# Kernel optimization log

Measured on AMD Instinct MI355X. Metric: run time of the kernel, lower is better.

## Reference

```python
import jax, jax.numpy as jnp
import numpy as np

NEG_INF = -1000000000.0
INPUT_SIZE = 1024
HIDDEN_SIZE = 64
B, S = 8, 2048


def setup_inputs() -> dict:
    key = jax.random.key(0)
    ks = jax.random.split(key, 8)
    scale = 1.0 / np.sqrt(INPUT_SIZE)
    inp = {
        "input": jax.random.normal(ks[0], (B, S, INPUT_SIZE), dtype=jnp.float32),
        "mask": jax.random.randint(ks[1], (B, S, S), 0, 2, dtype=jnp.int32),
        "W_q": jax.random.uniform(ks[2], (HIDDEN_SIZE, INPUT_SIZE), jnp.float32, -scale, scale),
        "b_q": jax.random.uniform(ks[3], (HIDDEN_SIZE,), jnp.float32, -scale, scale),
        "W_k": jax.random.uniform(ks[4], (HIDDEN_SIZE, INPUT_SIZE), jnp.float32, -scale, scale),
        "b_k": jax.random.uniform(ks[5], (HIDDEN_SIZE,), jnp.float32, -scale, scale),
        "W_v": jax.random.uniform(ks[6], (HIDDEN_SIZE, INPUT_SIZE), jnp.float32, -scale, scale),
        "b_v": jax.random.uniform(ks[7], (HIDDEN_SIZE,), jnp.float32, -scale, scale),
    }
    return inp


def reference(input, mask, W_q, b_q, W_k, b_k, W_v, b_v):
    inv_sqrt_d = 1.0 / np.sqrt(HIDDEN_SIZE)
    # Q/K/V projections: torch Linear is x @ W.T + b
    q = jnp.einsum('bsi,hi->bsh', input, W_q) + b_q  # (B,S,H)
    k = jnp.einsum('bsi,hi->bsh', input, W_k) + b_k
    v = jnp.einsum('bsi,hi->bsh', input, W_v) + b_v
    scores = jnp.einsum('bqh,bkh->bqk', q, k) * inv_sqrt_d  # (B,S,S)
    scores = jnp.where(mask == 0, NEG_INF, scores)
    probs = jax.nn.softmax(scores, axis=-1)
    return jnp.einsum('bqk,bkh->bqh', probs, v)  # (B,S,H)
```

## Files before the change

### kernel.cpp

```cpp
#include <hip/hip_runtime.h>

typedef __bf16 bf16;
typedef bf16 bf16x4 __attribute__((ext_vector_type(4)));
typedef bf16 bf16x8 __attribute__((ext_vector_type(8)));
typedef float floatx4 __attribute__((ext_vector_type(4)));
typedef unsigned int u32;
typedef unsigned long long u64;

#define B_ 8
#define S_ 2048
#define I_ 1024
#define H_ 64

__device__ __forceinline__ void async_cp16(bf16* lds_base, const bf16* g_base, int lane) {
    __builtin_amdgcn_global_load_lds(
        (const __attribute__((address_space(1))) u32*)(g_base + lane * 8),
        (__attribute__((address_space(3))) u32*)lds_base, 16, 0, 0);
}

__global__ void conv_w(const float* __restrict__ Wq, const float* __restrict__ bq,
                       const float* __restrict__ Wk, const float* __restrict__ bk,
                       const float* __restrict__ Wv, const float* __restrict__ bv,
                       bf16* __restrict__ Wc2, float* __restrict__ bc) {
    int idx = blockIdx.x * 256 + threadIdx.x;
    int n = idx >> 10, i = idx & 1023;
    float v;
    if (n < 64)       v = Wq[n * I_ + i] * 0.125f;
    else if (n < 128) v = Wk[(n - 64) * I_ + i];
    else              v = Wv[(n - 128) * I_ + i];
    int s = i >> 7, kl = i & 127;
    Wc2[(size_t)s * 26112 + n * 136 + kl] = (bf16)v;
    if (idx < 192) {
        float bb = (idx < 64) ? bq[idx] * 0.125f
                 : (idx < 128) ? bk[idx - 64] : bv[idx - 128];
        bc[idx] = bb;
    }
}

__global__ __launch_bounds__(256, 2) void qkv_gemm(const float* __restrict__ X,
                                                   const bf16* __restrict__ Wc2,
                                                   const float* __restrict__ bc,
                                                   bf16* __restrict__ Qd,
                                                   bf16* __restrict__ Kd2,
                                                   bf16* __restrict__ Vt2) {
    __shared__ __align__(16) bf16 Xs[32 * 136];
    __shared__ __align__(16) bf16 Ws[26112];

    int tid = threadIdx.x;
    int w = tid >> 6, lane = tid & 63;
    int n = lane & 15, g = lane >> 4;
    int m0 = blockIdx.x * 32;
    int mt = w & 1, nh = (w >> 1) * 96;

    floatx4 zero4 = {0.0f, 0.0f, 0.0f, 0.0f};
    floatx4 acc[6];
#pragma unroll
    for (int t = 0; t < 6; ++t) acc[t] = zero4;

    int xrow = tid >> 3, xcb = (tid & 7) * 16;
    const float* xsrc = X + (size_t)(m0 + xrow) * I_ + xcb;
    bf16* xdst = Xs + xrow * 136 + xcb;

    for (int s = 0; s < 8; ++s) {
        const float* xp = xsrc + s * 128;
        float4 x0 = *(const float4*)(xp);
        float4 x1 = *(const float4*)(xp + 4);
        float4 x2 = *(const float4*)(xp + 8);
        float4 x3 = *(const float4*)(xp + 12);
#pragma unroll
        for (int i = 0; i < 13; ++i) {
            int inst = i * 4 + w;
            if (inst < 51)
                async_cp16(Ws + inst * 512, Wc2 + (size_t)s * 26112 + inst * 512, lane);
        }
        bf16x8 b0, b1;
        b0[0] = (bf16)x0.x; b0[1] = (bf16)x0.y; b0[2] = (bf16)x0.z; b0[3] = (bf16)x0.w;
        b0[4] = (bf16)x1.x; b0[5] = (bf16)x1.y; b0[6] = (bf16)x1.z; b0[7] = (bf16)x1.w;
        b1[0] = (bf16)x2.x; b1[1] = (bf16)x2.y; b1[2] = (bf16)x2.z; b1[3] = (bf16)x2.w;
        b1[4] = (bf16)x3.x; b1[5] = (bf16)x3.y; b1[6] = (bf16)x3.z; b1[7] = (bf16)x3.w;
        *(bf16x8*)xdst = b0;
        *(bf16x8*)(xdst + 8) = b1;
        __syncthreads();

#pragma unroll
        for (int ks = 0; ks < 4; ++ks) {
            bf16x8 xa = *(bf16x8*)(Xs + (mt * 16 + n) * 136 + ks * 32 + g * 8);
#pragma unroll
            for (int nt = 0; nt < 6; ++nt) {
                bf16x8 wb = *(bf16x8*)(Ws + (nh + nt * 16 + n) * 136 + ks * 32 + g * 8);
                acc[nt] = __builtin_amdgcn_mfma_f32_16x16x32_bf16(xa, wb, acc[nt], 0, 0, 0);
            }
        }
        __syncthreads();
    }

    int b = m0 >> 11;
    int sb = (m0 & 2047) + mt * 16 + g * 4;
#pragma unroll
    for (int nt = 0; nt < 6; ++nt) {
        int ng = nh + nt * 16 + n;
        float bias = bc[ng];
        if (ng < 64) {
#pragma unroll
            for (int r = 0; r < 4; ++r)
                Qd[(size_t)(b * S_ + sb + r) * H_ + ng] = (bf16)(acc[nt][r] + bias);
        } else if (ng < 128) {
            int hc = (ng - 64) >> 3, j = (ng - 64) & 7;
#pragma unroll
            for (int r = 0; r < 4; ++r)
                Kd2[((size_t)(b * 8 + hc) * S_ + sb + r) * 8 + j] = (bf16)(acc[nt][r] + bias);
        } else {
            int hh = ng - 128, kc = sb >> 3, jj = sb & 7;
            bf16x4 pk;
#pragma unroll
            for (int r = 0; r < 4; ++r) pk[r] = (bf16)(acc[nt][r] + bias);
            *(bf16x4*)(Vt2 + ((size_t)(b * 256 + kc) * 64 + hh) * 8 + jj) = pk;
        }
    }
}

__global__ __launch_bounds__(256, 4) void attn(const bf16* __restrict__ Qd,
                                               const bf16* __restrict__ Kd2,
                                               const bf16* __restrict__ Vt2,
                                               const int* __restrict__ mask,
                                               float* __restrict__ po,
                                               float* __restrict__ pl) {
    __shared__ __align__(16) bf16 regA[8704];
    __shared__ __align__(16) bf16 Vs[16 * 528];
    __shared__ __align__(16) u32 bfm[64][4];

    int tid = threadIdx.x;
    int w = tid >> 6, lane = tid & 63;
    int n = lane & 15, g = lane >> 4;
    int bid = blockIdx.x;
    int ksp = bid & 3;
    int qt = (bid >> 2) & 31;
    int b = bid >> 7;
    int q0 = qt * 64;

    const bf16* qptr = Qd + (size_t)(b * S_ + q0 + w * 16 + n) * H_ + g * 8;
    bf16x8 qa0 = *(const bf16x8*)qptr;
    bf16x8 qa1 = *(const bf16x8*)(qptr + 32);

    floatx4 zero4 = {0.0f, 0.0f, 0.0f, 0.0f};
    floatx4 o[4];
#pragma unroll
    for (int t = 0; t < 4; ++t) o[t] = zero4;
    float l_i[4] = {0.0f, 0.0f, 0.0f, 0.0f};

    const int* msl = mask + (size_t)(b * S_ + q0 + w * 16) * S_ + lane;

    for (int kt = ksp * 4; kt < ksp * 4 + 4; ++kt) {
        int mv[16][2];
#pragma unroll
        for (int rr = 0; rr < 16; ++rr)
#pragma unroll
            for (int c = 0; c < 2; ++c)
                mv[rr][c] = msl[(size_t)rr * S_ + kt * 128 + c * 64];
#pragma unroll
        for (int j = 0; j < 4; ++j) {
            int hc = w * 2 + (j >> 1), p = j & 1;
            async_cp16(regA + hc * 1040 + p * 512,
                       Kd2 + ((size_t)(b * 8 + hc) * S_ + kt * 128 + p * 64) * 8, lane);
        }
#pragma unroll
        for (int j = 0; j < 4; ++j) {
            int kcl = w * 4 + j;
            async_cp16(Vs + kcl * 528,
                       Vt2 + ((size_t)(b * 256 + kt * 16 + kcl) * 64) * 8, lane);
        }
#pragma unroll
        for (int rr = 0; rr < 16; ++rr)
#pragma unroll
            for (int c = 0; c < 2; ++c) {
                u64 bits = __ballot(mv[rr][c] != 0);
                if (lane == 0) {
                    bfm[w * 16 + rr][c * 2]     = (u32)bits;
                    bfm[w * 16 + rr][c * 2 + 1] = (u32)(bits >> 32);
                }
            }
        __syncthreads();

        u32 mq[4][4];
#pragma unroll
        for (int r = 0; r < 4; ++r) {
            uint4 t4 = *(const uint4*)&bfm[w * 16 + g * 4 + r][0];
            mq[r][0] = t4.x; mq[r][1] = t4.y; mq[r][2] = t4.z; mq[r][3] = t4.w;
        }

        floatx4 s[8];
#pragma unroll
        for (int nt = 0; nt < 8; ++nt) {
            floatx4 a = zero4;
            a = __builtin_amdgcn_mfma_f32_16x16x32_bf16(
                    qa0, *(const bf16x8*)(regA + g * 1040 + (nt * 16 + n) * 8), a, 0, 0, 0);
            a = __builtin_amdgcn_mfma_f32_16x16x32_bf16(
                    qa1, *(const bf16x8*)(regA + (4 + g) * 1040 + (nt * 16 + n) * 8), a, 0, 0, 0);
            s[nt] = a;
        }

#pragma unroll
        for (int r = 0; r < 4; ++r)
#pragma unroll
            for (int nt = 0; nt < 8; ++nt) {
                float e = __expf(s[nt][r]);
                bool bit = (mq[r][nt >> 1] >> ((nt & 1) * 16 + n)) & 1u;
                float p = bit ? e : 0.0f;
                s[nt][r] = p;
                l_i[r] += p;
            }
        __syncthreads();

#pragma unroll
        for (int r = 0; r < 4; ++r)
#pragma unroll
            for (int nt = 0; nt < 8; ++nt)
                regA[(w * 16 + g * 4 + r) * 136 + nt * 16 + n] = (bf16)s[nt][r];
        __syncthreads();

#pragma unroll
        for (int k0 = 0; k0 < 4; ++k0) {
            bf16x8 pa = *(bf16x8*)(regA + (w * 16 + n) * 136 + k0 * 32 + g * 8);
#pragma unroll
            for (int ht = 0; ht < 4; ++ht) {
                bf16x8 vb = *(bf16x8*)(Vs + (k0 * 4 + g) * 528 + (ht * 16 + n) * 8);
                o[ht] = __builtin_amdgcn_mfma_f32_16x16x32_bf16(pa, vb, o[ht], 0, 0, 0);
            }
        }
        __syncthreads();
    }

#pragma unroll
    for (int r = 0; r < 4; ++r)
#pragma unroll
        for (int off = 1; off < 16; off <<= 1)
            l_i[r] += __shfl_xor(l_i[r], off, 64);

    float* pb = po + (size_t)bid * 4096;
#pragma unroll
    for (int ht = 0; ht < 4; ++ht)
#pragma unroll
        for (int r = 0; r < 4; ++r)
            pb[(w * 16 + g * 4 + r) * 64 + ht * 16 + n] = o[ht][r];
    if (n == 0) {
#pragma unroll
        for (int r = 0; r < 4; ++r)
            pl[(size_t)bid * 64 + w * 16 + g * 4 + r] = l_i[r];
    }
}

__global__ __launch_bounds__(256) void reduce_o(const float* __restrict__ po,
                                                const float* __restrict__ pl,
                                                float* __restrict__ out) {
    int idx = blockIdx.x * 256 + threadIdx.x;
    int h = idx & 63, q = idx >> 6;
    int b = q >> 11, qq = q & 2047;
    int qt = qq >> 6, ql = qq & 63;
    int bid0 = (b * 32 + qt) * 4;
    float num = 0.0f, den = 0.0f;
#pragma unroll
    for (int j = 0; j < 4; ++j) {
        den += pl[(size_t)(bid0 + j) * 64 + ql];
        num += po[(size_t)(bid0 + j) * 4096 + ql * 64 + h];
    }
    out[(size_t)q * 64 + h] = num / den;
}

extern "C" void kernel_launch(void* const* d_in, const int* in_sizes, int n_in,
                              void* d_out, int out_size, void* d_ws, size_t ws_size,
                              hipStream_t stream) {
    const float* X    = (const float*)d_in[0];
    const int*   mask = (const int*)d_in[1];
    const float* Wq   = (const float*)d_in[2];
    const float* bq   = (const float*)d_in[3];
    const float* Wk   = (const float*)d_in[4];
    const float* bk   = (const float*)d_in[5];
    const float* Wv   = (const float*)d_in[6];
    const float* bv   = (const float*)d_in[7];
    float* out = (float*)d_out;

    char* p = (char*)d_ws;
    bf16* Qd   = (bf16*)p;  p += (size_t)B_ * S_ * H_ * 2;
    bf16* Kd2  = (bf16*)p;  p += (size_t)B_ * S_ * H_ * 2;
    bf16* Vt2  = (bf16*)p;  p += (size_t)B_ * S_ * H_ * 2;
    bf16* Wc2  = (bf16*)p;  p += (size_t)8 * 26112 * 2;
    float* bc  = (float*)p; p += 1024;
    float* po  = (float*)p; p += (size_t)1024 * 4096 * 4;
    float* pl  = (float*)p; p += (size_t)1024 * 64 * 4;

    conv_w<<<dim3(768), dim3(256), 0, stream>>>(Wq, bq, Wk, bk, Wv, bv, Wc2, bc);
    qkv_gemm<<<dim3(512), dim3(256), 0, stream>>>(X, Wc2, bc, Qd, Kd2, Vt2);
    attn<<<dim3(1024), dim3(256), 0, stream>>>(Qd, Kd2, Vt2, mask, po, pl);
    reduce_o<<<dim3(4096), dim3(256), 0, stream>>>(po, pl, out);
}
```

Before: 272.6 us.

## Read weights and K/V fragments directly from global memory, drop LDS staging

```diff
diff --git a/kernel.cpp b/kernel.cpp
--- a/kernel.cpp
+++ b/kernel.cpp
@@ -12,24 +12,19 @@
 #define I_ 1024
 #define H_ 64
 
-__device__ __forceinline__ void async_cp16(bf16* lds_base, const bf16* g_base, int lane) {
-    __builtin_amdgcn_global_load_lds(
-        (const __attribute__((address_space(1))) u32*)(g_base + lane * 8),
-        (__attribute__((address_space(3))) u32*)lds_base, 16, 0, 0);
-}
-
 __global__ void conv_w(const float* __restrict__ Wq, const float* __restrict__ bq,
                        const float* __restrict__ Wk, const float* __restrict__ bk,
                        const float* __restrict__ Wv, const float* __restrict__ bv,
-                       bf16* __restrict__ Wc2, float* __restrict__ bc) {
+                       bf16* __restrict__ Wf, float* __restrict__ bc) {
     int idx = blockIdx.x * 256 + threadIdx.x;
-    int n = idx >> 10, i = idx & 1023;
+    int nrow = idx >> 10, i = idx & 1023;
     float v;
-    if (n < 64)       v = Wq[n * I_ + i] * 0.125f;
-    else if (n < 128) v = Wk[(n - 64) * I_ + i];
-    else              v = Wv[(n - 128) * I_ + i];
-    int s = i >> 7, kl = i & 127;
-    Wc2[(size_t)s * 26112 + n * 136 + kl] = (bf16)v;
+    if (nrow < 64)       v = Wq[nrow * I_ + i] * 0.125f;
+    else if (nrow < 128) v = Wk[(nrow - 64) * I_ + i];
+    else                 v = Wv[(nrow - 128) * I_ + i];
+    int kc = i >> 5, t = i & 31, g = t >> 3, j = t & 7;
+    int nt = nrow >> 4, nl = nrow & 15;
+    Wf[(size_t)(kc * 12 + nt) * 512 + (g * 16 + nl) * 8 + j] = (bf16)v;
     if (idx < 192) {
         float bb = (idx < 64) ? bq[idx] * 0.125f
                  : (idx < 128) ? bk[idx - 64] : bv[idx - 128];
@@ -37,68 +32,65 @@
     }
 }
 
-__global__ __launch_bounds__(256, 2) void qkv_gemm(const float* __restrict__ X,
-                                                   const bf16* __restrict__ Wc2,
-                                                   const float* __restrict__ bc,
-                                                   bf16* __restrict__ Qd,
-                                                   bf16* __restrict__ Kd2,
-                                                   bf16* __restrict__ Vt2) {
-    __shared__ __align__(16) bf16 Xs[32 * 136];
-    __shared__ __align__(16) bf16 Ws[26112];
-
-    int tid = threadIdx.x;
-    int w = tid >> 6, lane = tid & 63;
+__global__ __launch_bounds__(64) void qkv_gemm(const float* __restrict__ X,
+                                               const bf16* __restrict__ Wf,
+                                               const float* __restrict__ bc,
+                                               bf16* __restrict__ Qd,
+                                               bf16* __restrict__ Kd2,
+                                               bf16* __restrict__ Vt2) {
+    __shared__ __align__(16) bf16 Xs[16 * 136];
+
+    int lane = threadIdx.x;
     int n = lane & 15, g = lane >> 4;
-    int m0 = blockIdx.x * 32;
-    int mt = w & 1, nh = (w >> 1) * 96;
+    int m0 = blockIdx.x * 16;
 
     floatx4 zero4 = {0.0f, 0.0f, 0.0f, 0.0f};
-    floatx4 acc[6];
-#pragma unroll
-    for (int t = 0; t < 6; ++t) acc[t] = zero4;
-
-    int xrow = tid >> 3, xcb = (tid & 7) * 16;
-    const float* xsrc = X + (size_t)(m0 + xrow) * I_ + xcb;
-    bf16* xdst = Xs + xrow * 136 + xcb;
+    floatx4 acc[12];
+#pragma unroll
+    for (int t = 0; t < 12; ++t) acc[t] = zero4;
+
+    const float* xb = X + (size_t)m0 * I_;
+
+    float4 xr[8];
+#pragma unroll
+    for (int q = 0; q < 8; ++q) {
+        int f = q * 256 + lane * 4;
+        xr[q] = *(const float4*)(xb + (size_t)(f >> 7) * I_ + (f & 127));
+    }
 
     for (int s = 0; s < 8; ++s) {
-        const float* xp = xsrc + s * 128;
-        float4 x0 = *(const float4*)(xp);
-        float4 x1 = *(const float4*)(xp + 4);
-        float4 x2 = *(const float4*)(xp + 8);
-        float4 x3 = *(const float4*)(xp + 12);
-#pragma unroll
-        for (int i = 0; i < 13; ++i) {
-            int inst = i * 4 + w;
-            if (inst < 51)
-                async_cp16(Ws + inst * 512, Wc2 + (size_t)s * 26112 + inst * 512, lane);
-        }
-        bf16x8 b0, b1;
-        b0[0] = (bf16)x0.x; b0[1] = (bf16)x0.y; b0[2] = (bf16)x0.z; b0[3] = (bf16)x0.w;
-        b0[4] = (bf16)x1.x; b0[5] = (bf16)x1.y; b0[6] = (bf16)x1.z; b0[7] = (bf16)x1.w;
-        b1[0] = (bf16)x2.x; b1[1] = (bf16)x2.y; b1[2] = (bf16)x2.z; b1[3] = (bf16)x2.w;
-        b1[4] = (bf16)x3.x; b1[5] = (bf16)x3.y; b1[6] = (bf16)x3.z; b1[7] = (bf16)x3.w;
-        *(bf16x8*)xdst = b0;
-        *(bf16x8*)(xdst + 8) = b1;
-        __syncthreads();
-
+#pragma unroll
+        for (int q = 0; q < 8; ++q) {
+            int f = q * 256 + lane * 4;
+            bf16x4 xv;
+            xv[0] = (bf16)xr[q].x; xv[1] = (bf16)xr[q].y;
+            xv[2] = (bf16)xr[q].z; xv[3] = (bf16)xr[q].w;
+            *(bf16x4*)(Xs + (f >> 7) * 136 + (f & 127)) = xv;
+        }
+        if (s < 7) {
+#pragma unroll
+            for (int q = 0; q < 8; ++q) {
+                int f = q * 256 + lane * 4;
+                xr[q] = *(const float4*)(xb + (size_t)(f >> 7) * I_ + (s + 1) * 128 + (f & 127));
+            }
+        }
 #pragma unroll
         for (int ks = 0; ks < 4; ++ks) {
-            bf16x8 xa = *(bf16x8*)(Xs + (mt * 16 + n) * 136 + ks * 32 + g * 8);
-#pragma unroll
-            for (int nt = 0; nt < 6; ++nt) {
-                bf16x8 wb = *(bf16x8*)(Ws + (nh + nt * 16 + n) * 136 + ks * 32 + g * 8);
+            bf16x8 xa = *(bf16x8*)(Xs + n * 136 + ks * 32 + g * 8);
+            const bf16* wrow = Wf + (size_t)((s * 4 + ks) * 12) * 512 + lane * 8;
+#pragma unroll
+            for (int nt = 0; nt < 12; ++nt) {
+                bf16x8 wb = *(const bf16x8*)(wrow + nt * 512);
                 acc[nt] = __builtin_amdgcn_mfma_f32_16x16x32_bf16(xa, wb, acc[nt], 0, 0, 0);
             }
         }
-        __syncthreads();
     }
 
     int b = m0 >> 11;
-    int sb = (m0 & 2047) + mt * 16 + g * 4;
-#pragma unroll
-    for (int nt = 0; nt < 6; ++nt) {
-        int ng = nh + nt * 16 + n;
+    int sb = (m0 & 2047) + g * 4;
+#pragma unroll
+    for (int nt = 0; nt < 12; ++nt) {
+        int ng = nt * 16 + n;
         float bias = bc[ng];
         if (ng < 64) {
 #pragma unroll
@@ -119,15 +111,13 @@
     }
 }
 
-__global__ __launch_bounds__(256, 4) void attn(const bf16* __restrict__ Qd,
+__global__ __launch_bounds__(256, 2) void attn(const bf16* __restrict__ Qd,
                                                const bf16* __restrict__ Kd2,
                                                const bf16* __restrict__ Vt2,
                                                const int* __restrict__ mask,
                                                float* __restrict__ po,
                                                float* __restrict__ pl) {
-    __shared__ __align__(16) bf16 regA[8704];
-    __shared__ __align__(16) bf16 Vs[16 * 528];
-    __shared__ __align__(16) u32 bfm[64][4];
+    __shared__ __align__(16) bf16 Ps[64 * 136];
 
     int tid = threadIdx.x;
     int w = tid >> 6, lane = tid & 63;
@@ -149,6 +139,9 @@
     float l_i[4] = {0.0f, 0.0f, 0.0f, 0.0f};
 
     const int* msl = mask + (size_t)(b * S_ + q0 + w * 16) * S_ + lane;
+    const bf16* kp0 = Kd2 + (size_t)(b * 8 + g) * S_ * 8;
+    const bf16* kp1 = Kd2 + (size_t)(b * 8 + 4 + g) * S_ * 8;
+    const bf16* vp  = Vt2 + (size_t)(b * 256) * 512;
 
     for (int kt = ksp * 4; kt < ksp * 4 + 4; ++kt) {
         int mv[16][2];
@@ -157,46 +150,33 @@
 #pragma unroll
             for (int c = 0; c < 2; ++c)
                 mv[rr][c] = msl[(size_t)rr * S_ + kt * 128 + c * 64];
-#pragma unroll
-        for (int j = 0; j < 4; ++j) {
-            int hc = w * 2 + (j >> 1), p = j & 1;
-            async_cp16(regA + hc * 1040 + p * 512,
-                       Kd2 + ((size_t)(b * 8 + hc) * S_ + kt * 128 + p * 64) * 8, lane);
-        }
-#pragma unroll
-        for (int j = 0; j < 4; ++j) {
-            int kcl = w * 4 + j;
-            async_cp16(Vs + kcl * 528,
-                       Vt2 + ((size_t)(b * 256 + kt * 16 + kcl) * 64) * 8, lane);
-        }
-#pragma unroll
-        for (int rr = 0; rr < 16; ++rr)
-#pragma unroll
-            for (int c = 0; c < 2; ++c) {
-                u64 bits = __ballot(mv[rr][c] != 0);
-                if (lane == 0) {
-                    bfm[w * 16 + rr][c * 2]     = (u32)bits;
-                    bfm[w * 16 + rr][c * 2 + 1] = (u32)(bits >> 32);
-                }
-            }
-        __syncthreads();
-
+
+        floatx4 s[8];
+#pragma unroll
+        for (int nt = 0; nt < 8; ++nt) {
+            bf16x8 k0 = *(const bf16x8*)(kp0 + (size_t)(kt * 128 + nt * 16 + n) * 8);
+            bf16x8 k1 = *(const bf16x8*)(kp1 + (size_t)(kt * 128 + nt * 16 + n) * 8);
+            floatx4 a = zero4;
+            a = __builtin_amdgcn_mfma_f32_16x16x32_bf16(qa0, k0, a, 0, 0, 0);
+            a = __builtin_amdgcn_mfma_f32_16x16x32_bf16(qa1, k1, a, 0, 0, 0);
+            s[nt] = a;
+        }
+
+        u64 bal0[16], bal1[16];
+#pragma unroll
+        for (int rr = 0; rr < 16; ++rr) {
+            bal0[rr] = __ballot(mv[rr][0] != 0);
+            bal1[rr] = __ballot(mv[rr][1] != 0);
+        }
         u32 mq[4][4];
 #pragma unroll
         for (int r = 0; r < 4; ++r) {
-            uint4 t4 = *(const uint4*)&bfm[w * 16 + g * 4 + r][0];
-            mq[r][0] = t4.x; mq[r][1] = t4.y; mq[r][2] = t4.z; mq[r][3] = t4.w;
-        }
-
-        floatx4 s[8];
-#pragma unroll
-        for (int nt = 0; nt < 8; ++nt) {
-            floatx4 a = zero4;
-            a = __builtin_amdgcn_mfma_f32_16x16x32_bf16(
-                    qa0, *(const bf16x8*)(regA + g * 1040 + (nt * 16 + n) * 8), a, 0, 0, 0);
-            a = __builtin_amdgcn_mfma_f32_16x16x32_bf16(
-                    qa1, *(const bf16x8*)(regA + (4 + g) * 1040 + (nt * 16 + n) * 8), a, 0, 0, 0);
-            s[nt] = a;
+            u64 s0 = (g == 0) ? bal0[r] : (g == 1) ? bal0[4 + r]
+                   : (g == 2) ? bal0[8 + r] : bal0[12 + r];
+            u64 s1 = (g == 0) ? bal1[r] : (g == 1) ? bal1[4 + r]
+                   : (g == 2) ? bal1[8 + r] : bal1[12 + r];
+            mq[r][0] = (u32)s0; mq[r][1] = (u32)(s0 >> 32);
+            mq[r][2] = (u32)s1; mq[r][3] = (u32)(s1 >> 32);
         }
 
 #pragma unroll
@@ -209,25 +189,23 @@
                 s[nt][r] = p;
                 l_i[r] += p;
             }
-        __syncthreads();
 
 #pragma unroll
         for (int r = 0; r < 4; ++r)
 #pragma unroll
             for (int nt = 0; nt < 8; ++nt)
-                regA[(w * 16 + g * 4 + r) * 136 + nt * 16 + n] = (bf16)s[nt][r];
-        __syncthreads();
+                Ps[(w * 16 + g * 4 + r) * 136 + nt * 16 + n] = (bf16)s[nt][r];
 
 #pragma unroll
         for (int k0 = 0; k0 < 4; ++k0) {
-            bf16x8 pa = *(bf16x8*)(regA + (w * 16 + n) * 136 + k0 * 32 + g * 8);
+            bf16x8 pa = *(bf16x8*)(Ps + (w * 16 + n) * 136 + k0 * 32 + g * 8);
 #pragma unroll
             for (int ht = 0; ht < 4; ++ht) {
-                bf16x8 vb = *(bf16x8*)(Vs + (k0 * 4 + g) * 528 + (ht * 16 + n) * 8);
+                bf16x8 vb = *(const bf16x8*)(vp +
+                    ((size_t)(kt * 16 + k0 * 4 + g) * 64 + ht * 16 + n) * 8);
                 o[ht] = __builtin_amdgcn_mfma_f32_16x16x32_bf16(pa, vb, o[ht], 0, 0, 0);
             }
         }
-        __syncthreads();
     }
 
 #pragma unroll
@@ -283,13 +261,13 @@
     bf16* Qd   = (bf16*)p;  p += (size_t)B_ * S_ * H_ * 2;
     bf16* Kd2  = (bf16*)p;  p += (size_t)B_ * S_ * H_ * 2;
     bf16* Vt2  = (bf16*)p;  p += (size_t)B_ * S_ * H_ * 2;
-    bf16* Wc2  = (bf16*)p;  p += (size_t)8 * 26112 * 2;
+    bf16* Wf   = (bf16*)p;  p += (size_t)192 * 1024 * 2;
     float* bc  = (float*)p; p += 1024;
     float* po  = (float*)p; p += (size_t)1024 * 4096 * 4;
     float* pl  = (float*)p; p += (size_t)1024 * 64 * 4;
 
-    conv_w<<<dim3(768), dim3(256), 0, stream>>>(Wq, bq, Wk, bk, Wv, bv, Wc2, bc);
-    qkv_gemm<<<dim3(512), dim3(256), 0, stream>>>(X, Wc2, bc, Qd, Kd2, Vt2);
+    conv_w<<<dim3(768), dim3(256), 0, stream>>>(Wq, bq, Wk, bk, Wv, bv, Wf, bc);
+    qkv_gemm<<<dim3(1024), dim3(64), 0, stream>>>(X, Wf, bc, Qd, Kd2, Vt2);
     attn<<<dim3(1024), dim3(256), 0, stream>>>(Qd, Kd2, Vt2, mask, po, pl);
     reduce_o<<<dim3(4096), dim3(256), 0, stream>>>(po, pl, out);
 }
```

Result: slower. 278.3 us (+2.1%).
